# Performance work log

Measured on AMD Instinct MI355X. Metric: run time of the kernel, lower is better.

Reference implementation:

```python
import jax, jax.numpy as jnp
import numpy as np

B, S, D = 16, 2048, 128

def setup_inputs() -> dict:
    key = jax.random.key(0)
    k1, k2, k3, k4 = jax.random.split(key, 4)
    q = jax.random.normal(k1, (B, S, D), dtype=jnp.float32)
    k = jax.random.normal(k2, (B, S, D), dtype=jnp.float32)
    v = jax.random.normal(k3, (B, S, D), dtype=jnp.float32)
    scale = jnp.float32(1.0 / np.sqrt(D))
    attn_mask = jax.random.randint(k4, (B, S, S), 0, 2).astype(jnp.bool_)
    return {"q": q, "k": k, "v": v, "scale": scale, "attn_mask": attn_mask}

def reference(q, k, v, scale, attn_mask):
    # attention scores: [B, Sq, Sk]
    scores = jnp.einsum('bqd,bkd->bqk', q, k) * scale
    # masked_fill(attn_mask, -inf): True positions are masked out
    scores = jnp.where(attn_mask, -jnp.inf, scores)
    attention = jax.nn.softmax(scores, axis=2)
    # dropout prob = 0.0 -> identity
    context = jnp.einsum('bqk,bkd->bqd', attention, v)
    return (context, attention)
```

## Files before the change

kernel.cpp:

```cpp
#include <hip/hip_runtime.h>
#include <hip/hip_bf16.h>
#include <hip/hip_fp16.h>

#define B_ 16
#define S_ 2048
#define D_ 128
#define QB 64
#define KT 64
#define NT_ 32

typedef __attribute__((ext_vector_type(8))) short short8;
typedef __attribute__((ext_vector_type(8))) unsigned short u16x8;
typedef __attribute__((ext_vector_type(4))) float f32x4;
typedef __attribute__((ext_vector_type(4))) float f32x4v;
typedef __attribute__((ext_vector_type(4))) int i32x4;
typedef __attribute__((ext_vector_type(4))) unsigned short u16x4;

__device__ __forceinline__ unsigned short f2bf(float f) {
  unsigned int u = __builtin_bit_cast(unsigned int, f);
  unsigned int r = (u + 0x7fffu + ((u >> 16) & 1u)) >> 16;
  return (unsigned short)r;
}
__device__ __forceinline__ float bf2f(unsigned short h) {
  return __builtin_bit_cast(float, (unsigned int)h << 16);
}
__device__ __forceinline__ int swz_bid(int bid, int nwg) {
  int cpx = nwg >> 3;
  return (bid & 7) * cpx + (bid >> 3);
}

__global__ void cvt_bf16_kernel(const float* __restrict__ x,
                                unsigned short* __restrict__ y,
                                const float* __restrict__ sc, int n4) {
  int i = blockIdx.x * blockDim.x + threadIdx.x;
  if (i >= n4) return;
  float s = sc ? sc[0] : 1.0f;
  float4 f = reinterpret_cast<const float4*>(x)[i];
  u16x4 o;
  o[0] = f2bf(f.x * s); o[1] = f2bf(f.y * s);
  o[2] = f2bf(f.z * s); o[3] = f2bf(f.w * s);
  reinterpret_cast<u16x4*>(y)[i] = o;
}

__global__ void vtrans_kernel(const float* __restrict__ v,
                              unsigned short* __restrict__ vT) {
  __shared__ float tile[32][33];
  int b = blockIdx.z, kt = blockIdx.x, dt = blockIdx.y;
  int t = threadIdx.x;
  int c = t & 31, r0 = t >> 5;
  const float* src = v + ((size_t)b * S_ + (size_t)kt * 32) * D_ + dt * 32;
#pragma unroll
  for (int i = 0; i < 4; i++) {
    int r = r0 + 8 * i;
    tile[r][c] = src[(size_t)r * D_ + c];
  }
  __syncthreads();
  unsigned short* dst = vT + ((size_t)b * D_ + dt * 32) * S_ + (size_t)kt * 32;
#pragma unroll
  for (int i = 0; i < 4; i++) {
    int r = r0 + 8 * i;
    dst[(size_t)r * S_ + c] = f2bf(tile[c][r]);
  }
}

__global__ __launch_bounds__(512, 4)
void attn_main_kernel(const unsigned short* __restrict__ qbf,
                      const unsigned short* __restrict__ kbf,
                      const unsigned short* __restrict__ vTb,
                      const void* __restrict__ maskp,
                      float* __restrict__ ctx,
                      float* __restrict__ att) {
  __shared__ __align__(16) char kbuf[2][KT * 256];
  __shared__ __align__(16) char vbuf[2][D_ * 128];
  __shared__ __align__(16) char etile[QB * 128];
  __shared__ float zpart[8][2][16];
  __shared__ float iz_l[QB];

  const int tid = threadIdx.x;
  const int bid = swz_bid(blockIdx.x, B_ * (S_ / QB));
  const int b  = bid >> 5;
  const int q0 = (bid & 31) << 6;

  const int w   = tid >> 6;
  const int l   = tid & 63;
  const int l16 = l & 15;
  const int lq  = l >> 4;
  const int qh  = w & 1;
  const int kq  = w >> 1;

  int myv = 0;
  if (tid < 256) myv = (reinterpret_cast<const unsigned int*>(maskp)[tid] > 1u) ? 1 : 0;
  const int mask_is_byte = __syncthreads_or(myv);

  const char* kbb = reinterpret_cast<const char*>(kbf + (((size_t)b * S_) << 7));
  const char* vbb = reinterpret_cast<const char*>(vTb + ((size_t)b * D_) * S_);
  const unsigned char* mask8 = reinterpret_cast<const unsigned char*>(maskp);
  const int* mask32 = reinterpret_cast<const int*>(maskp);
  size_t mrowq[2];
#pragma unroll
  for (int qg = 0; qg < 2; ++qg)
    mrowq[qg] = ((size_t)b * S_ + q0 + qh * 32 + qg * 16 + l16) * S_ + kq * 16 + lq * 4;

  short8 qf[2][4];
#pragma unroll
  for (int qg = 0; qg < 2; ++qg) {
    const unsigned short* qp =
        qbf + (((size_t)(b * S_ + q0 + qh * 32 + qg * 16 + l16)) << 7) + lq * 8;
#pragma unroll
    for (int ks = 0; ks < 4; ks++)
      qf[qg][ks] = *reinterpret_cast<const short8*>(qp + ks * 32);
  }

  const int krow_s = tid >> 3, kcol_s = (tid & 7) * 32;
  const int vrow_s = tid >> 2, vcol_s = (tid & 3) * 32;
  const size_t ksrc_off = (size_t)krow_s * 256 + kcol_s;
  const size_t vsrc_off = (size_t)vrow_s * (S_ * 2) + vcol_s;
  const int kswz = (krow_s & 15) << 4, vswz = (vrow_s & 7) << 4;

  u16x8 stk0, stk1, stv0, stv1;
  stk0 = *reinterpret_cast<const u16x8*>(kbb + ksrc_off);
  stk1 = *reinterpret_cast<const u16x8*>(kbb + ksrc_off + 16);
  {
    char* kd = &kbuf[0][0] + krow_s * 256;
    *reinterpret_cast<u16x8*>(kd + (kcol_s ^ kswz)) = stk0;
    *reinterpret_cast<u16x8*>(kd + ((kcol_s + 16) ^ kswz)) = stk1;
  }
  __syncthreads();

  unsigned int mbits[8] = {0, 0, 0, 0, 0, 0, 0, 0};
  float Zl[2] = {0.0f, 0.0f};
  const int krow_f = kq * 16 + l16;
  const int kfx = (krow_f & 15) << 4;

  for (int t = 0; t < NT_; ++t) {
    const int cur = t & 1;
    if (t < NT_ - 1) {
      const char* src = kbb + ((size_t)(t + 1) * KT * 256);
      stk0 = *reinterpret_cast<const u16x8*>(src + ksrc_off);
      stk1 = *reinterpret_cast<const u16x8*>(src + ksrc_off + 16);
    }
    unsigned int nib[2];
    if (mask_is_byte) {
#pragma unroll
      for (int qg = 0; qg < 2; ++qg) {
        unsigned int mv = *reinterpret_cast<const unsigned int*>(
            mask8 + mrowq[qg] + t * KT);
        nib[qg] = ((mv & 0x000000ffu) ? 1u : 0u) | ((mv & 0x0000ff00u) ? 2u : 0u) |
                  ((mv & 0x00ff0000u) ? 4u : 0u) | ((mv & 0xff000000u) ? 8u : 0u);
      }
    } else {
#pragma unroll
      for (int qg = 0; qg < 2; ++qg) {
        i32x4 mi = *reinterpret_cast<const i32x4*>(mask32 + mrowq[qg] + t * KT);
        nib[qg] = (mi[0] ? 1u : 0u) | (mi[1] ? 2u : 0u) |
                  (mi[2] ? 4u : 0u) | (mi[3] ? 8u : 0u);
      }
    }
    mbits[t >> 2] |= (nib[0] | (nib[1] << 4)) << ((t & 3) * 8);

    const char* kp = &kbuf[cur][0] + krow_f * 256;
    f32x4 a0 = {0.f, 0.f, 0.f, 0.f}, a1 = {0.f, 0.f, 0.f, 0.f};
#pragma unroll
    for (int ks = 0; ks < 4; ++ks) {
      short8 kfr = *reinterpret_cast<const short8*>(kp + ((ks * 64 + lq * 16) ^ kfx));
      a0 = __builtin_amdgcn_mfma_f32_16x16x32_bf16(kfr, qf[0][ks], a0, 0, 0, 0);
      a1 = __builtin_amdgcn_mfma_f32_16x16x32_bf16(kfr, qf[1][ks], a1, 0, 0, 0);
    }
#pragma unroll
    for (int r = 0; r < 4; ++r) {
      if (!(nib[0] & (1u << r))) Zl[0] += __expf(a0[r]);
      if (!(nib[1] & (1u << r))) Zl[1] += __expf(a1[r]);
    }
    if (t < NT_ - 1) {
      char* kd = &kbuf[cur ^ 1][0] + krow_s * 256;
      *reinterpret_cast<u16x8*>(kd + (kcol_s ^ kswz)) = stk0;
      *reinterpret_cast<u16x8*>(kd + ((kcol_s + 16) ^ kswz)) = stk1;
    }
    __syncthreads();
  }

  stk0 = *reinterpret_cast<const u16x8*>(kbb + ksrc_off);
  stk1 = *reinterpret_cast<const u16x8*>(kbb + ksrc_off + 16);
  stv0 = *reinterpret_cast<const u16x8*>(vbb + vsrc_off);
  stv1 = *reinterpret_cast<const u16x8*>(vbb + vsrc_off + 16);
#pragma unroll
  for (int qg = 0; qg < 2; ++qg) {
    Zl[qg] += __shfl_xor(Zl[qg], 16, 64);
    Zl[qg] += __shfl_xor(Zl[qg], 32, 64);
  }
  if (lq == 0) { zpart[w][0][l16] = Zl[0]; zpart[w][1][l16] = Zl[1]; }
  __syncthreads();
  if (tid < QB) {
    const int qh_ = tid >> 5, qg_ = (tid >> 4) & 1, r_ = tid & 15;
    float Z = 0.0f;
#pragma unroll
    for (int kk = 0; kk < 4; ++kk) Z += zpart[kk * 2 + qh_][qg_][r_];
    iz_l[tid] = 1.0f / Z;
  }
  {
    char* kd = &kbuf[0][0] + krow_s * 256;
    *reinterpret_cast<u16x8*>(kd + (kcol_s ^ kswz)) = stk0;
    *reinterpret_cast<u16x8*>(kd + ((kcol_s + 16) ^ kswz)) = stk1;
    char* vd = &vbuf[0][0] + vrow_s * 128;
    *reinterpret_cast<u16x8*>(vd + (vcol_s ^ vswz)) = stv0;
    *reinterpret_cast<u16x8*>(vd + ((vcol_s + 16) ^ vswz)) = stv1;
  }
  __syncthreads();

  const float izA = iz_l[w * 8 + (l >> 4)];
  const float izB = iz_l[w * 8 + 4 + (l >> 4)];

  f32x4 apv[2][2] = {{{0.f,0.f,0.f,0.f},{0.f,0.f,0.f,0.f}},
                     {{0.f,0.f,0.f,0.f},{0.f,0.f,0.f,0.f}}};
  for (int t = 0; t < NT_; ++t) {
    const int cur = t & 1;
    if (t < NT_ - 1) {
      const char* src = kbb + ((size_t)(t + 1) * KT * 256);
      stk0 = *reinterpret_cast<const u16x8*>(src + ksrc_off);
      stk1 = *reinterpret_cast<const u16x8*>(src + ksrc_off + 16);
      const char* vs2 = vbb + (size_t)(t + 1) * 128;
      stv0 = *reinterpret_cast<const u16x8*>(vs2 + vsrc_off);
      stv1 = *reinterpret_cast<const u16x8*>(vs2 + vsrc_off + 16);
    }
    const char* kp = &kbuf[cur][0] + krow_f * 256;
    f32x4 a0 = {0.f, 0.f, 0.f, 0.f}, a1 = {0.f, 0.f, 0.f, 0.f};
#pragma unroll
    for (int ks = 0; ks < 4; ++ks) {
      short8 kfr = *reinterpret_cast<const short8*>(kp + ((ks * 64 + lq * 16) ^ kfx));
      a0 = __builtin_amdgcn_mfma_f32_16x16x32_bf16(kfr, qf[0][ks], a0, 0, 0, 0);
      a1 = __builtin_amdgcn_mfma_f32_16x16x32_bf16(kfr, qf[1][ks], a1, 0, 0, 0);
    }
    const unsigned int nibs = mbits[t >> 2] >> ((t & 3) * 8);
    u16x4 eb[2];
#pragma unroll
    for (int r = 0; r < 4; ++r) {
      eb[0][r] = f2bf((nibs & (1u << r)) ? 0.0f : __expf(a0[r]));
      eb[1][r] = f2bf((nibs & (16u << r)) ? 0.0f : __expf(a1[r]));
    }
    __syncthreads();
#pragma unroll
    for (int qg = 0; qg < 2; ++qg) {
      const int re = qh * 32 + qg * 16 + l16;
      *reinterpret_cast<u16x4*>(
          etile + re * 128 + ((kq * 32 + lq * 8) ^ ((re & 7) << 4))) = eb[qg];
    }
    if (t < NT_ - 1) {
      char* kd = &kbuf[cur ^ 1][0] + krow_s * 256;
      *reinterpret_cast<u16x8*>(kd + (kcol_s ^ kswz)) = stk0;
      *reinterpret_cast<u16x8*>(kd + ((kcol_s + 16) ^ kswz)) = stk1;
      char* vd = &vbuf[cur ^ 1][0] + vrow_s * 128;
      *reinterpret_cast<u16x8*>(vd + (vcol_s ^ vswz)) = stv0;
      *reinterpret_cast<u16x8*>(vd + ((vcol_s + 16) ^ vswz)) = stv1;
    }
    __syncthreads();
#pragma unroll
    for (int h = 0; h < 2; ++h) {
      const int re = w * 8 + h * 4 + (l >> 4);
      const float iz = h ? izB : izA;
      u16x4 ev = *reinterpret_cast<const u16x4*>(
          etile + re * 128 + (((l & 15) * 8) ^ ((re & 7) << 4)));
      f32x4v pv;
#pragma unroll
      for (int j = 0; j < 4; ++j) pv[j] = bf2f(ev[j]) * iz;
      __builtin_nontemporal_store(pv, reinterpret_cast<f32x4v*>(
          att + ((size_t)(b * S_ + q0 + re)) * S_ + t * KT + (l & 15) * 4));
    }
#pragma unroll
    for (int qg = 0; qg < 2; ++qg) {
      const int re = qh * 32 + qg * 16 + l16;
      const char* ep = etile + re * 128;
      const int ex = (re & 7) << 4;
#pragma unroll
      for (int dg = 0; dg < 2; ++dg) {
        const int vr = kq * 32 + dg * 16 + l16;
        const char* vp = &vbuf[cur][0] + vr * 128;
        const int vx = (vr & 7) << 4;
#pragma unroll
        for (int kk = 0; kk < 2; ++kk) {
          short8 afr = *reinterpret_cast<const short8*>(ep + ((kk * 64 + lq * 16) ^ ex));
          short8 bfr = *reinterpret_cast<const short8*>(vp + ((kk * 64 + lq * 16) ^ vx));
          apv[qg][dg] = __builtin_amdgcn_mfma_f32_16x16x32_bf16(afr, bfr, apv[qg][dg], 0, 0, 0);
        }
      }
    }
  }

#pragma unroll
  for (int qg = 0; qg < 2; ++qg) {
#pragma unroll
    for (int dg = 0; dg < 2; ++dg) {
#pragma unroll
      for (int r = 0; r < 4; ++r) {
        const float izr = iz_l[qh * 32 + qg * 16 + lq * 4 + r];
        __builtin_nontemporal_store(
            apv[qg][dg][r] * izr,
            ctx + ((size_t)(b * S_ + q0 + qh * 32 + qg * 16 + lq * 4 + r)) * D_ +
                kq * 32 + dg * 16 + l16);
      }
    }
  }
}

extern "C" void kernel_launch(void* const* d_in, const int* in_sizes, int n_in,
                              void* d_out, int out_size, void* d_ws, size_t ws_size,
                              hipStream_t stream) {
  (void)in_sizes; (void)n_in; (void)out_size; (void)ws_size;
  const float* q = (const float*)d_in[0];
  const float* k = (const float*)d_in[1];
  const float* v = (const float*)d_in[2];
  const float* scale = (const float*)d_in[3];
  const void* mask = d_in[4];

  const size_t qkv_elems = (size_t)B_ * S_ * D_;
  unsigned short* qbf = (unsigned short*)d_ws;
  unsigned short* kbf = qbf + qkv_elems;
  unsigned short* vTb = kbf + qkv_elems;

  float* ctx = (float*)d_out;
  float* att = ctx + (size_t)B_ * S_ * D_;

  const int n4 = B_ * S_ * D_ / 4;
  cvt_bf16_kernel<<<dim3((n4 + 255) / 256), dim3(256), 0, stream>>>(q, qbf, scale, n4);
  cvt_bf16_kernel<<<dim3((n4 + 255) / 256), dim3(256), 0, stream>>>(k, kbf, nullptr, n4);
  vtrans_kernel<<<dim3(S_ / 32, D_ / 32, B_), dim3(256), 0, stream>>>(v, vTb);
  attn_main_kernel<<<dim3(B_ * (S_ / QB)), dim3(512), 0, stream>>>(
      qbf, kbf, vTb, mask, ctx, att);
}
```

Before: 162.7 us.

## Precompute packed mask bits and load K/V fragments directly from global

Adds a separate kernel that packs the boolean mask into 64-bit nibble words per query row and key tile, so the main kernel reads compact bits instead of the raw mask on each pass. The main kernel halves the query block to 32 rows with 256 threads and drops the LDS staging of K and V. Each wave now loads its MFMA fragments straight from global memory with register prefetch. Normalization moves into the exp step before bf16 rounding, which removes the per-store scaling of context. The trade-off is a lower-bandwidth mask read against redundant global loads of K and V, an extra kernel launch and extra workspace use.

```diff
diff --git a/kernel.cpp b/kernel.cpp
--- a/kernel.cpp
+++ b/kernel.cpp
@@ -5,7 +5,7 @@
 #define B_ 16
 #define S_ 2048
 #define D_ 128
-#define QB 64
+#define QB 32
 #define KT 64
 #define NT_ 32
 
@@ -63,126 +63,117 @@
   }
 }
 
-__global__ __launch_bounds__(512, 4)
+__global__ void masknib_kernel(const void* __restrict__ maskp,
+                               unsigned long long* __restrict__ mnib) {
+  const int tid = threadIdx.x;
+  int myv = (reinterpret_cast<const unsigned int*>(maskp)[tid] > 1u) ? 1 : 0;
+  const int mask_is_byte = __syncthreads_or(myv);
+  const size_t i = (size_t)blockIdx.x * 256 + tid;
+  const int t = i & 31;
+  const int q = (i >> 5) & 2047;
+  const int b = i >> 16;
+  const size_t base = ((size_t)(b * S_ + q)) * S_ + t * 64;
+  unsigned long long out = 0;
+  if (mask_is_byte) {
+    const unsigned char* m8 = reinterpret_cast<const unsigned char*>(maskp) + base;
+#pragma unroll
+    for (int c4 = 0; c4 < 16; ++c4) {
+      unsigned int v = *reinterpret_cast<const unsigned int*>(m8 + c4 * 4);
+      unsigned long long nib = ((v & 0x000000ffu) ? 1u : 0u) |
+                               ((v & 0x0000ff00u) ? 2u : 0u) |
+                               ((v & 0x00ff0000u) ? 4u : 0u) |
+                               ((v & 0xff000000u) ? 8u : 0u);
+      out |= nib << (4 * c4);
+    }
+  } else {
+    const int* m32 = reinterpret_cast<const int*>(maskp) + base;
+#pragma unroll
+    for (int c4 = 0; c4 < 16; ++c4) {
+      i32x4 mi = *reinterpret_cast<const i32x4*>(m32 + c4 * 4);
+      unsigned long long nib = (mi[0] ? 1u : 0u) | (mi[1] ? 2u : 0u) |
+                               (mi[2] ? 4u : 0u) | (mi[3] ? 8u : 0u);
+      out |= nib << (4 * c4);
+    }
+  }
+  mnib[i] = out;
+}
+
+__global__ __launch_bounds__(256, 4)
 void attn_main_kernel(const unsigned short* __restrict__ qbf,
                       const unsigned short* __restrict__ kbf,
                       const unsigned short* __restrict__ vTb,
-                      const void* __restrict__ maskp,
+                      const unsigned long long* __restrict__ mnib,
                       float* __restrict__ ctx,
                       float* __restrict__ att) {
-  __shared__ __align__(16) char kbuf[2][KT * 256];
-  __shared__ __align__(16) char vbuf[2][D_ * 128];
   __shared__ __align__(16) char etile[QB * 128];
-  __shared__ float zpart[8][2][16];
+  __shared__ float zpart[4][2][16];
   __shared__ float iz_l[QB];
 
   const int tid = threadIdx.x;
   const int bid = swz_bid(blockIdx.x, B_ * (S_ / QB));
-  const int b  = bid >> 5;
-  const int q0 = (bid & 31) << 6;
+  const int b  = bid >> 6;
+  const int q0 = (bid & 63) << 5;
 
   const int w   = tid >> 6;
   const int l   = tid & 63;
   const int l16 = l & 15;
   const int lq  = l >> 4;
-  const int qh  = w & 1;
-  const int kq  = w >> 1;
-
-  int myv = 0;
-  if (tid < 256) myv = (reinterpret_cast<const unsigned int*>(maskp)[tid] > 1u) ? 1 : 0;
-  const int mask_is_byte = __syncthreads_or(myv);
-
-  const char* kbb = reinterpret_cast<const char*>(kbf + (((size_t)b * S_) << 7));
-  const char* vbb = reinterpret_cast<const char*>(vTb + ((size_t)b * D_) * S_);
-  const unsigned char* mask8 = reinterpret_cast<const unsigned char*>(maskp);
-  const int* mask32 = reinterpret_cast<const int*>(maskp);
-  size_t mrowq[2];
-#pragma unroll
-  for (int qg = 0; qg < 2; ++qg)
-    mrowq[qg] = ((size_t)b * S_ + q0 + qh * 32 + qg * 16 + l16) * S_ + kq * 16 + lq * 4;
 
   short8 qf[2][4];
 #pragma unroll
   for (int qg = 0; qg < 2; ++qg) {
     const unsigned short* qp =
-        qbf + (((size_t)(b * S_ + q0 + qh * 32 + qg * 16 + l16)) << 7) + lq * 8;
+        qbf + (((size_t)(b * S_ + q0 + qg * 16 + l16)) << 7) + lq * 8;
 #pragma unroll
     for (int ks = 0; ks < 4; ks++)
       qf[qg][ks] = *reinterpret_cast<const short8*>(qp + ks * 32);
   }
 
-  const int krow_s = tid >> 3, kcol_s = (tid & 7) * 32;
-  const int vrow_s = tid >> 2, vcol_s = (tid & 3) * 32;
-  const size_t ksrc_off = (size_t)krow_s * 256 + kcol_s;
-  const size_t vsrc_off = (size_t)vrow_s * (S_ * 2) + vcol_s;
-  const int kswz = (krow_s & 15) << 4, vswz = (vrow_s & 7) << 4;
-
-  u16x8 stk0, stk1, stv0, stv1;
-  stk0 = *reinterpret_cast<const u16x8*>(kbb + ksrc_off);
-  stk1 = *reinterpret_cast<const u16x8*>(kbb + ksrc_off + 16);
+  const unsigned long long* mp0 =
+      mnib + ((size_t)(b * S_ + q0 + l16)) * NT_;
+  const unsigned long long* mp1 =
+      mnib + ((size_t)(b * S_ + q0 + 16 + l16)) * NT_;
+  const int nsh = (w * 4 + lq) * 4;
+
+  const char* kbb = reinterpret_cast<const char*>(kbf) + ((size_t)b * S_) * 256;
+  const char* vbb = reinterpret_cast<const char*>(vTb) + ((size_t)b * D_) * (S_ * 2);
+
+  short8 kc[4], kn[4];
   {
-    char* kd = &kbuf[0][0] + krow_s * 256;
-    *reinterpret_cast<u16x8*>(kd + (kcol_s ^ kswz)) = stk0;
-    *reinterpret_cast<u16x8*>(kd + ((kcol_s + 16) ^ kswz)) = stk1;
-  }
-  __syncthreads();
-
-  unsigned int mbits[8] = {0, 0, 0, 0, 0, 0, 0, 0};
+    const char* kp = kbb + ((size_t)(w * 16 + l16)) * 256 + lq * 16;
+#pragma unroll
+    for (int ks = 0; ks < 4; ++ks)
+      kc[ks] = *reinterpret_cast<const short8*>(kp + ks * 64);
+  }
+  unsigned long long mc0 = mp0[0], mc1 = mp1[0], mn0, mn1;
   float Zl[2] = {0.0f, 0.0f};
-  const int krow_f = kq * 16 + l16;
-  const int kfx = (krow_f & 15) << 4;
-
   for (int t = 0; t < NT_; ++t) {
-    const int cur = t & 1;
-    if (t < NT_ - 1) {
-      const char* src = kbb + ((size_t)(t + 1) * KT * 256);
-      stk0 = *reinterpret_cast<const u16x8*>(src + ksrc_off);
-      stk1 = *reinterpret_cast<const u16x8*>(src + ksrc_off + 16);
-    }
-    unsigned int nib[2];
-    if (mask_is_byte) {
-#pragma unroll
-      for (int qg = 0; qg < 2; ++qg) {
-        unsigned int mv = *reinterpret_cast<const unsigned int*>(
-            mask8 + mrowq[qg] + t * KT);
-        nib[qg] = ((mv & 0x000000ffu) ? 1u : 0u) | ((mv & 0x0000ff00u) ? 2u : 0u) |
-                  ((mv & 0x00ff0000u) ? 4u : 0u) | ((mv & 0xff000000u) ? 8u : 0u);
-      }
-    } else {
-#pragma unroll
-      for (int qg = 0; qg < 2; ++qg) {
-        i32x4 mi = *reinterpret_cast<const i32x4*>(mask32 + mrowq[qg] + t * KT);
-        nib[qg] = (mi[0] ? 1u : 0u) | (mi[1] ? 2u : 0u) |
-                  (mi[2] ? 4u : 0u) | (mi[3] ? 8u : 0u);
-      }
-    }
-    mbits[t >> 2] |= (nib[0] | (nib[1] << 4)) << ((t & 3) * 8);
-
-    const char* kp = &kbuf[cur][0] + krow_f * 256;
+    if (t + 1 < NT_) {
+      const char* kp = kbb + ((size_t)((t + 1) * KT + w * 16 + l16)) * 256 + lq * 16;
+#pragma unroll
+      for (int ks = 0; ks < 4; ++ks)
+        kn[ks] = *reinterpret_cast<const short8*>(kp + ks * 64);
+      mn0 = mp0[t + 1];
+      mn1 = mp1[t + 1];
+    }
     f32x4 a0 = {0.f, 0.f, 0.f, 0.f}, a1 = {0.f, 0.f, 0.f, 0.f};
 #pragma unroll
     for (int ks = 0; ks < 4; ++ks) {
-      short8 kfr = *reinterpret_cast<const short8*>(kp + ((ks * 64 + lq * 16) ^ kfx));
-      a0 = __builtin_amdgcn_mfma_f32_16x16x32_bf16(kfr, qf[0][ks], a0, 0, 0, 0);
-      a1 = __builtin_amdgcn_mfma_f32_16x16x32_bf16(kfr, qf[1][ks], a1, 0, 0, 0);
-    }
+      a0 = __builtin_amdgcn_mfma_f32_16x16x32_bf16(kc[ks], qf[0][ks], a0, 0, 0, 0);
+      a1 = __builtin_amdgcn_mfma_f32_16x16x32_bf16(kc[ks], qf[1][ks], a1, 0, 0, 0);
+    }
+    const unsigned int n0 = (unsigned int)(mc0 >> nsh) & 15u;
+    const unsigned int n1 = (unsigned int)(mc1 >> nsh) & 15u;
 #pragma unroll
     for (int r = 0; r < 4; ++r) {
-      if (!(nib[0] & (1u << r))) Zl[0] += __expf(a0[r]);
-      if (!(nib[1] & (1u << r))) Zl[1] += __expf(a1[r]);
-    }
-    if (t < NT_ - 1) {
-      char* kd = &kbuf[cur ^ 1][0] + krow_s * 256;
-      *reinterpret_cast<u16x8*>(kd + (kcol_s ^ kswz)) = stk0;
-      *reinterpret_cast<u16x8*>(kd + ((kcol_s + 16) ^ kswz)) = stk1;
-    }
-    __syncthreads();
-  }
-
-  stk0 = *reinterpret_cast<const u16x8*>(kbb + ksrc_off);
-  stk1 = *reinterpret_cast<const u16x8*>(kbb + ksrc_off + 16);
-  stv0 = *reinterpret_cast<const u16x8*>(vbb + vsrc_off);
-  stv1 = *reinterpret_cast<const u16x8*>(vbb + vsrc_off + 16);
+      if (!((n0 >> r) & 1u)) Zl[0] += __expf(a0[r]);
+      if (!((n1 >> r) & 1u)) Zl[1] += __expf(a1[r]);
+    }
+#pragma unroll
+    for (int ks = 0; ks < 4; ++ks) kc[ks] = kn[ks];
+    mc0 = mn0; mc1 = mn1;
+  }
+
 #pragma unroll
   for (int qg = 0; qg < 2; ++qg) {
     Zl[qg] += __shfl_xor(Zl[qg], 16, 64);
@@ -191,98 +182,93 @@
   if (lq == 0) { zpart[w][0][l16] = Zl[0]; zpart[w][1][l16] = Zl[1]; }
   __syncthreads();
   if (tid < QB) {
-    const int qh_ = tid >> 5, qg_ = (tid >> 4) & 1, r_ = tid & 15;
-    float Z = 0.0f;
-#pragma unroll
-    for (int kk = 0; kk < 4; ++kk) Z += zpart[kk * 2 + qh_][qg_][r_];
+    const int qg_ = tid >> 4, r_ = tid & 15;
+    float Z = zpart[0][qg_][r_] + zpart[1][qg_][r_] +
+              zpart[2][qg_][r_] + zpart[3][qg_][r_];
     iz_l[tid] = 1.0f / Z;
   }
-  {
-    char* kd = &kbuf[0][0] + krow_s * 256;
-    *reinterpret_cast<u16x8*>(kd + (kcol_s ^ kswz)) = stk0;
-    *reinterpret_cast<u16x8*>(kd + ((kcol_s + 16) ^ kswz)) = stk1;
-    char* vd = &vbuf[0][0] + vrow_s * 128;
-    *reinterpret_cast<u16x8*>(vd + (vcol_s ^ vswz)) = stv0;
-    *reinterpret_cast<u16x8*>(vd + ((vcol_s + 16) ^ vswz)) = stv1;
-  }
   __syncthreads();
-
-  const float izA = iz_l[w * 8 + (l >> 4)];
-  const float izB = iz_l[w * 8 + 4 + (l >> 4)];
+  const float izq0 = iz_l[l16];
+  const float izq1 = iz_l[16 + l16];
 
   f32x4 apv[2][2] = {{{0.f,0.f,0.f,0.f},{0.f,0.f,0.f,0.f}},
                      {{0.f,0.f,0.f,0.f},{0.f,0.f,0.f,0.f}}};
+  {
+    const char* kp = kbb + ((size_t)(w * 16 + l16)) * 256 + lq * 16;
+#pragma unroll
+    for (int ks = 0; ks < 4; ++ks)
+      kc[ks] = *reinterpret_cast<const short8*>(kp + ks * 64);
+  }
+  mc0 = mp0[0]; mc1 = mp1[0];
   for (int t = 0; t < NT_; ++t) {
-    const int cur = t & 1;
-    if (t < NT_ - 1) {
-      const char* src = kbb + ((size_t)(t + 1) * KT * 256);
-      stk0 = *reinterpret_cast<const u16x8*>(src + ksrc_off);
-      stk1 = *reinterpret_cast<const u16x8*>(src + ksrc_off + 16);
-      const char* vs2 = vbb + (size_t)(t + 1) * 128;
-      stv0 = *reinterpret_cast<const u16x8*>(vs2 + vsrc_off);
-      stv1 = *reinterpret_cast<const u16x8*>(vs2 + vsrc_off + 16);
-    }
-    const char* kp = &kbuf[cur][0] + krow_f * 256;
+    short8 bv[2][2];
+#pragma unroll
+    for (int dg = 0; dg < 2; ++dg) {
+      const char* vp = vbb + ((size_t)(w * 32 + dg * 16 + l16)) * (S_ * 2)
+                           + (t * 64 + lq * 8) * 2;
+#pragma unroll
+      for (int kk = 0; kk < 2; ++kk)
+        bv[dg][kk] = *reinterpret_cast<const short8*>(vp + kk * 64);
+    }
+    if (t + 1 < NT_) {
+      const char* kp = kbb + ((size_t)((t + 1) * KT + w * 16 + l16)) * 256 + lq * 16;
+#pragma unroll
+      for (int ks = 0; ks < 4; ++ks)
+        kn[ks] = *reinterpret_cast<const short8*>(kp + ks * 64);
+      mn0 = mp0[t + 1];
+      mn1 = mp1[t + 1];
+    }
     f32x4 a0 = {0.f, 0.f, 0.f, 0.f}, a1 = {0.f, 0.f, 0.f, 0.f};
 #pragma unroll
     for (int ks = 0; ks < 4; ++ks) {
-      short8 kfr = *reinterpret_cast<const short8*>(kp + ((ks * 64 + lq * 16) ^ kfx));
-      a0 = __builtin_amdgcn_mfma_f32_16x16x32_bf16(kfr, qf[0][ks], a0, 0, 0, 0);
-      a1 = __builtin_amdgcn_mfma_f32_16x16x32_bf16(kfr, qf[1][ks], a1, 0, 0, 0);
-    }
-    const unsigned int nibs = mbits[t >> 2] >> ((t & 3) * 8);
-    u16x4 eb[2];
+      a0 = __builtin_amdgcn_mfma_f32_16x16x32_bf16(kc[ks], qf[0][ks], a0, 0, 0, 0);
+      a1 = __builtin_amdgcn_mfma_f32_16x16x32_bf16(kc[ks], qf[1][ks], a1, 0, 0, 0);
+    }
+    const unsigned int n0 = (unsigned int)(mc0 >> nsh) & 15u;
+    const unsigned int n1 = (unsigned int)(mc1 >> nsh) & 15u;
+    u16x4 eb0, eb1;
 #pragma unroll
     for (int r = 0; r < 4; ++r) {
-      eb[0][r] = f2bf((nibs & (1u << r)) ? 0.0f : __expf(a0[r]));
-      eb[1][r] = f2bf((nibs & (16u << r)) ? 0.0f : __expf(a1[r]));
+      float p0 = ((n0 >> r) & 1u) ? 0.0f : __expf(a0[r]) * izq0;
+      float p1 = ((n1 >> r) & 1u) ? 0.0f : __expf(a1[r]) * izq1;
+      eb0[r] = f2bf(p0);
+      eb1[r] = f2bf(p1);
     }
     __syncthreads();
+    {
+      const int c = w * 32 + lq * 8;
+      const int r0_ = l16, r1_ = 16 + l16;
+      *reinterpret_cast<u16x4*>(etile + r0_ * 128 + (c ^ ((r0_ & 7) << 4))) = eb0;
+      *reinterpret_cast<u16x4*>(etile + r1_ * 128 + (c ^ ((r1_ & 7) << 4))) = eb1;
+    }
+    __syncthreads();
+    {
+      const int re = w * 8 + (l >> 3);
+      const int cb = (l & 7) * 16;
+      u16x8 ev = *reinterpret_cast<const u16x8*>(
+          etile + re * 128 + (cb ^ ((re & 7) << 4)));
+      f32x4v o0, o1;
+#pragma unroll
+      for (int j = 0; j < 4; ++j) { o0[j] = bf2f(ev[j]); o1[j] = bf2f(ev[j + 4]); }
+      float* ap = att + ((size_t)(b * S_ + q0 + re)) * S_ + t * 64 + (l & 7) * 8;
+      __builtin_nontemporal_store(o0, reinterpret_cast<f32x4v*>(ap));
+      __builtin_nontemporal_store(o1, reinterpret_cast<f32x4v*>(ap) + 1);
+    }
 #pragma unroll
     for (int qg = 0; qg < 2; ++qg) {
-      const int re = qh * 32 + qg * 16 + l16;
-      *reinterpret_cast<u16x4*>(
-          etile + re * 128 + ((kq * 32 + lq * 8) ^ ((re & 7) << 4))) = eb[qg];
-    }
-    if (t < NT_ - 1) {
-      char* kd = &kbuf[cur ^ 1][0] + krow_s * 256;
-      *reinterpret_cast<u16x8*>(kd + (kcol_s ^ kswz)) = stk0;
-      *reinterpret_cast<u16x8*>(kd + ((kcol_s + 16) ^ kswz)) = stk1;
-      char* vd = &vbuf[cur ^ 1][0] + vrow_s * 128;
-      *reinterpret_cast<u16x8*>(vd + (vcol_s ^ vswz)) = stv0;
-      *reinterpret_cast<u16x8*>(vd + ((vcol_s + 16) ^ vswz)) = stv1;
-    }
-    __syncthreads();
-#pragma unroll
-    for (int h = 0; h < 2; ++h) {
-      const int re = w * 8 + h * 4 + (l >> 4);
-      const float iz = h ? izB : izA;
-      u16x4 ev = *reinterpret_cast<const u16x4*>(
-          etile + re * 128 + (((l & 15) * 8) ^ ((re & 7) << 4)));
-      f32x4v pv;
-#pragma unroll
-      for (int j = 0; j < 4; ++j) pv[j] = bf2f(ev[j]) * iz;
-      __builtin_nontemporal_store(pv, reinterpret_cast<f32x4v*>(
-          att + ((size_t)(b * S_ + q0 + re)) * S_ + t * KT + (l & 15) * 4));
-    }
-#pragma unroll
-    for (int qg = 0; qg < 2; ++qg) {
-      const int re = qh * 32 + qg * 16 + l16;
-      const char* ep = etile + re * 128;
-      const int ex = (re & 7) << 4;
-#pragma unroll
-      for (int dg = 0; dg < 2; ++dg) {
-        const int vr = kq * 32 + dg * 16 + l16;
-        const char* vp = &vbuf[cur][0] + vr * 128;
-        const int vx = (vr & 7) << 4;
-#pragma unroll
-        for (int kk = 0; kk < 2; ++kk) {
-          short8 afr = *reinterpret_cast<const short8*>(ep + ((kk * 64 + lq * 16) ^ ex));
-          short8 bfr = *reinterpret_cast<const short8*>(vp + ((kk * 64 + lq * 16) ^ vx));
-          apv[qg][dg] = __builtin_amdgcn_mfma_f32_16x16x32_bf16(afr, bfr, apv[qg][dg], 0, 0, 0);
-        }
+      const int rq = qg * 16 + l16;
+      const char* ep = etile + rq * 128;
+      const int ex = (rq & 7) << 4;
+#pragma unroll
+      for (int kk = 0; kk < 2; ++kk) {
+        short8 afr = *reinterpret_cast<const short8*>(ep + ((kk * 64 + lq * 16) ^ ex));
+        apv[qg][0] = __builtin_amdgcn_mfma_f32_16x16x32_bf16(afr, bv[0][kk], apv[qg][0], 0, 0, 0);
+        apv[qg][1] = __builtin_amdgcn_mfma_f32_16x16x32_bf16(afr, bv[1][kk], apv[qg][1], 0, 0, 0);
       }
     }
+#pragma unroll
+    for (int ks = 0; ks < 4; ++ks) kc[ks] = kn[ks];
+    mc0 = mn0; mc1 = mn1;
   }
 
 #pragma unroll
@@ -291,11 +277,10 @@
     for (int dg = 0; dg < 2; ++dg) {
 #pragma unroll
       for (int r = 0; r < 4; ++r) {
-        const float izr = iz_l[qh * 32 + qg * 16 + lq * 4 + r];
         __builtin_nontemporal_store(
-            apv[qg][dg][r] * izr,
-            ctx + ((size_t)(b * S_ + q0 + qh * 32 + qg * 16 + lq * 4 + r)) * D_ +
-                kq * 32 + dg * 16 + l16);
+            apv[qg][dg][r],
+            ctx + ((size_t)(b * S_ + q0 + qg * 16 + lq * 4 + r)) * D_ +
+                w * 32 + dg * 16 + l16);
       }
     }
   }
@@ -315,6 +300,8 @@
   unsigned short* qbf = (unsigned short*)d_ws;
   unsigned short* kbf = qbf + qkv_elems;
   unsigned short* vTb = kbf + qkv_elems;
+  unsigned long long* mnib =
+      (unsigned long long*)(vTb + qkv_elems);
 
   float* ctx = (float*)d_out;
   float* att = ctx + (size_t)B_ * S_ * D_;
@@ -323,6 +310,7 @@
   cvt_bf16_kernel<<<dim3((n4 + 255) / 256), dim3(256), 0, stream>>>(q, qbf, scale, n4);
   cvt_bf16_kernel<<<dim3((n4 + 255) / 256), dim3(256), 0, stream>>>(k, kbf, nullptr, n4);
   vtrans_kernel<<<dim3(S_ / 32, D_ / 32, B_), dim3(256), 0, stream>>>(v, vTb);
-  attn_main_kernel<<<dim3(B_ * (S_ / QB)), dim3(512), 0, stream>>>(
-      qbf, kbf, vTb, mask, ctx, att);
-}
+  masknib_kernel<<<dim3(B_ * S_ * NT_ / 256), dim3(256), 0, stream>>>(mask, mnib);
+  attn_main_kernel<<<dim3(B_ * (S_ / QB)), dim3(256), 0, stream>>>(
+      qbf, kbf, vTb, mnib, ctx, att);
+}
```

Result: slower. 345.0 us (+112.1%).

## Precompute packed mask bits in a separate kernel and fold normalization into exp

Applied to the files above, without the earlier changes.

A new pre-pass kernel reads the boolean mask once and packs it into 64-bit bitmasks, one per query row and key tile, stored in workspace. The main kernel then loads one 64-bit word per row per tile in both passes instead of reading raw mask bytes, and drops the per-thread mbits register array. The inverse normalizer is now applied before the bf16 rounding of the exponentials, so the attention-matrix store and the context epilogue no longer scale. This costs an extra kernel launch and a 16 MB bitmask round trip, in exchange for lighter mask traffic and lower register use in the main kernel. Rounding after scaling also changes numerics slightly.

```diff
diff --git a/kernel.cpp b/kernel.cpp
--- a/kernel.cpp
+++ b/kernel.cpp
@@ -63,11 +63,46 @@
   }
 }
 
+__global__ void masknib_kernel(const void* __restrict__ maskp,
+                               unsigned long long* __restrict__ mnib) {
+  const int tid = threadIdx.x;
+  int myv = (reinterpret_cast<const unsigned int*>(maskp)[tid] > 1u) ? 1 : 0;
+  const int mask_is_byte = __syncthreads_or(myv);
+  const size_t i = (size_t)blockIdx.x * 256 + tid;
+  const int t = i & 31;
+  const int q = (i >> 5) & 2047;
+  const int b = i >> 16;
+  const size_t base = ((size_t)(b * S_ + q)) * S_ + t * 64;
+  unsigned long long out = 0;
+  if (mask_is_byte) {
+    const unsigned char* m8 = reinterpret_cast<const unsigned char*>(maskp) + base;
+#pragma unroll
+    for (int c4 = 0; c4 < 16; ++c4) {
+      unsigned int v = *reinterpret_cast<const unsigned int*>(m8 + c4 * 4);
+      unsigned long long nib = ((v & 0x000000ffu) ? 1u : 0u) |
+                               ((v & 0x0000ff00u) ? 2u : 0u) |
+                               ((v & 0x00ff0000u) ? 4u : 0u) |
+                               ((v & 0xff000000u) ? 8u : 0u);
+      out |= nib << (4 * c4);
+    }
+  } else {
+    const int* m32 = reinterpret_cast<const int*>(maskp) + base;
+#pragma unroll
+    for (int c4 = 0; c4 < 16; ++c4) {
+      i32x4 mi = *reinterpret_cast<const i32x4*>(m32 + c4 * 4);
+      unsigned long long nib = (mi[0] ? 1u : 0u) | (mi[1] ? 2u : 0u) |
+                               (mi[2] ? 4u : 0u) | (mi[3] ? 8u : 0u);
+      out |= nib << (4 * c4);
+    }
+  }
+  mnib[i] = out;
+}
+
 __global__ __launch_bounds__(512, 4)
 void attn_main_kernel(const unsigned short* __restrict__ qbf,
                       const unsigned short* __restrict__ kbf,
                       const unsigned short* __restrict__ vTb,
-                      const void* __restrict__ maskp,
+                      const unsigned long long* __restrict__ mnib,
                       float* __restrict__ ctx,
                       float* __restrict__ att) {
   __shared__ __align__(16) char kbuf[2][KT * 256];
@@ -88,19 +123,6 @@
   const int qh  = w & 1;
   const int kq  = w >> 1;
 
-  int myv = 0;
-  if (tid < 256) myv = (reinterpret_cast<const unsigned int*>(maskp)[tid] > 1u) ? 1 : 0;
-  const int mask_is_byte = __syncthreads_or(myv);
-
-  const char* kbb = reinterpret_cast<const char*>(kbf + (((size_t)b * S_) << 7));
-  const char* vbb = reinterpret_cast<const char*>(vTb + ((size_t)b * D_) * S_);
-  const unsigned char* mask8 = reinterpret_cast<const unsigned char*>(maskp);
-  const int* mask32 = reinterpret_cast<const int*>(maskp);
-  size_t mrowq[2];
-#pragma unroll
-  for (int qg = 0; qg < 2; ++qg)
-    mrowq[qg] = ((size_t)b * S_ + q0 + qh * 32 + qg * 16 + l16) * S_ + kq * 16 + lq * 4;
-
   short8 qf[2][4];
 #pragma unroll
   for (int qg = 0; qg < 2; ++qg) {
@@ -110,6 +132,15 @@
     for (int ks = 0; ks < 4; ks++)
       qf[qg][ks] = *reinterpret_cast<const short8*>(qp + ks * 32);
   }
+
+  const unsigned long long* mp0 =
+      mnib + ((size_t)(b * S_ + q0 + qh * 32 + l16)) * NT_;
+  const unsigned long long* mp1 =
+      mnib + ((size_t)(b * S_ + q0 + qh * 32 + 16 + l16)) * NT_;
+  const int nsh = kq * 16 + lq * 4;
+
+  const char* kbb = reinterpret_cast<const char*>(kbf + (((size_t)b * S_) << 7));
+  const char* vbb = reinterpret_cast<const char*>(vTb + ((size_t)b * D_) * S_);
 
   const int krow_s = tid >> 3, kcol_s = (tid & 7) * 32;
   const int vrow_s = tid >> 2, vcol_s = (tid & 3) * 32;
@@ -127,10 +158,10 @@
   }
   __syncthreads();
 
-  unsigned int mbits[8] = {0, 0, 0, 0, 0, 0, 0, 0};
   float Zl[2] = {0.0f, 0.0f};
   const int krow_f = kq * 16 + l16;
   const int kfx = (krow_f & 15) << 4;
+  unsigned long long mc0 = mp0[0], mc1 = mp1[0], mn0 = 0, mn1 = 0;
 
   for (int t = 0; t < NT_; ++t) {
     const int cur = t & 1;
@@ -138,26 +169,9 @@
       const char* src = kbb + ((size_t)(t + 1) * KT * 256);
       stk0 = *reinterpret_cast<const u16x8*>(src + ksrc_off);
       stk1 = *reinterpret_cast<const u16x8*>(src + ksrc_off + 16);
-    }
-    unsigned int nib[2];
-    if (mask_is_byte) {
-#pragma unroll
-      for (int qg = 0; qg < 2; ++qg) {
-        unsigned int mv = *reinterpret_cast<const unsigned int*>(
-            mask8 + mrowq[qg] + t * KT);
-        nib[qg] = ((mv & 0x000000ffu) ? 1u : 0u) | ((mv & 0x0000ff00u) ? 2u : 0u) |
-                  ((mv & 0x00ff0000u) ? 4u : 0u) | ((mv & 0xff000000u) ? 8u : 0u);
-      }
-    } else {
-#pragma unroll
-      for (int qg = 0; qg < 2; ++qg) {
-        i32x4 mi = *reinterpret_cast<const i32x4*>(mask32 + mrowq[qg] + t * KT);
-        nib[qg] = (mi[0] ? 1u : 0u) | (mi[1] ? 2u : 0u) |
-                  (mi[2] ? 4u : 0u) | (mi[3] ? 8u : 0u);
-      }
-    }
-    mbits[t >> 2] |= (nib[0] | (nib[1] << 4)) << ((t & 3) * 8);
-
+      mn0 = mp0[t + 1];
+      mn1 = mp1[t + 1];
+    }
     const char* kp = &kbuf[cur][0] + krow_f * 256;
     f32x4 a0 = {0.f, 0.f, 0.f, 0.f}, a1 = {0.f, 0.f, 0.f, 0.f};
 #pragma unroll
@@ -166,16 +180,19 @@
       a0 = __builtin_amdgcn_mfma_f32_16x16x32_bf16(kfr, qf[0][ks], a0, 0, 0, 0);
       a1 = __builtin_amdgcn_mfma_f32_16x16x32_bf16(kfr, qf[1][ks], a1, 0, 0, 0);
     }
+    const unsigned int n0 = (unsigned int)(mc0 >> nsh) & 15u;
+    const unsigned int n1 = (unsigned int)(mc1 >> nsh) & 15u;
 #pragma unroll
     for (int r = 0; r < 4; ++r) {
-      if (!(nib[0] & (1u << r))) Zl[0] += __expf(a0[r]);
-      if (!(nib[1] & (1u << r))) Zl[1] += __expf(a1[r]);
+      if (!((n0 >> r) & 1u)) Zl[0] += __expf(a0[r]);
+      if (!((n1 >> r) & 1u)) Zl[1] += __expf(a1[r]);
     }
     if (t < NT_ - 1) {
       char* kd = &kbuf[cur ^ 1][0] + krow_s * 256;
       *reinterpret_cast<u16x8*>(kd + (kcol_s ^ kswz)) = stk0;
       *reinterpret_cast<u16x8*>(kd + ((kcol_s + 16) ^ kswz)) = stk1;
     }
+    mc0 = mn0; mc1 = mn1;
     __syncthreads();
   }
 
@@ -207,11 +224,12 @@
   }
   __syncthreads();
 
-  const float izA = iz_l[w * 8 + (l >> 4)];
-  const float izB = iz_l[w * 8 + 4 + (l >> 4)];
+  const float izq0 = iz_l[qh * 32 + l16];
+  const float izq1 = iz_l[qh * 32 + 16 + l16];
 
   f32x4 apv[2][2] = {{{0.f,0.f,0.f,0.f},{0.f,0.f,0.f,0.f}},
                      {{0.f,0.f,0.f,0.f},{0.f,0.f,0.f,0.f}}};
+  mc0 = mp0[0]; mc1 = mp1[0];
   for (int t = 0; t < NT_; ++t) {
     const int cur = t & 1;
     if (t < NT_ - 1) {
@@ -221,6 +239,8 @@
       const char* vs2 = vbb + (size_t)(t + 1) * 128;
       stv0 = *reinterpret_cast<const u16x8*>(vs2 + vsrc_off);
       stv1 = *reinterpret_cast<const u16x8*>(vs2 + vsrc_off + 16);
+      mn0 = mp0[t + 1];
+      mn1 = mp1[t + 1];
     }
     const char* kp = &kbuf[cur][0] + krow_f * 256;
     f32x4 a0 = {0.f, 0.f, 0.f, 0.f}, a1 = {0.f, 0.f, 0.f, 0.f};
@@ -230,12 +250,13 @@
       a0 = __builtin_amdgcn_mfma_f32_16x16x32_bf16(kfr, qf[0][ks], a0, 0, 0, 0);
       a1 = __builtin_amdgcn_mfma_f32_16x16x32_bf16(kfr, qf[1][ks], a1, 0, 0, 0);
     }
-    const unsigned int nibs = mbits[t >> 2] >> ((t & 3) * 8);
+    const unsigned int n0 = (unsigned int)(mc0 >> nsh) & 15u;
+    const unsigned int n1 = (unsigned int)(mc1 >> nsh) & 15u;
     u16x4 eb[2];
 #pragma unroll
     for (int r = 0; r < 4; ++r) {
-      eb[0][r] = f2bf((nibs & (1u << r)) ? 0.0f : __expf(a0[r]));
-      eb[1][r] = f2bf((nibs & (16u << r)) ? 0.0f : __expf(a1[r]));
+      eb[0][r] = f2bf(((n0 >> r) & 1u) ? 0.0f : __expf(a0[r]) * izq0);
+      eb[1][r] = f2bf(((n1 >> r) & 1u) ? 0.0f : __expf(a1[r]) * izq1);
     }
     __syncthreads();
 #pragma unroll
@@ -252,16 +273,16 @@
       *reinterpret_cast<u16x8*>(vd + (vcol_s ^ vswz)) = stv0;
       *reinterpret_cast<u16x8*>(vd + ((vcol_s + 16) ^ vswz)) = stv1;
     }
+    mc0 = mn0; mc1 = mn1;
     __syncthreads();
 #pragma unroll
     for (int h = 0; h < 2; ++h) {
       const int re = w * 8 + h * 4 + (l >> 4);
-      const float iz = h ? izB : izA;
       u16x4 ev = *reinterpret_cast<const u16x4*>(
           etile + re * 128 + (((l & 15) * 8) ^ ((re & 7) << 4)));
       f32x4v pv;
 #pragma unroll
-      for (int j = 0; j < 4; ++j) pv[j] = bf2f(ev[j]) * iz;
+      for (int j = 0; j < 4; ++j) pv[j] = bf2f(ev[j]);
       __builtin_nontemporal_store(pv, reinterpret_cast<f32x4v*>(
           att + ((size_t)(b * S_ + q0 + re)) * S_ + t * KT + (l & 15) * 4));
     }
@@ -291,9 +312,8 @@
     for (int dg = 0; dg < 2; ++dg) {
 #pragma unroll
       for (int r = 0; r < 4; ++r) {
-        const float izr = iz_l[qh * 32 + qg * 16 + lq * 4 + r];
         __builtin_nontemporal_store(
-            apv[qg][dg][r] * izr,
+            apv[qg][dg][r],
             ctx + ((size_t)(b * S_ + q0 + qh * 32 + qg * 16 + lq * 4 + r)) * D_ +
                 kq * 32 + dg * 16 + l16);
       }
@@ -315,6 +335,8 @@
   unsigned short* qbf = (unsigned short*)d_ws;
   unsigned short* kbf = qbf + qkv_elems;
   unsigned short* vTb = kbf + qkv_elems;
+  unsigned long long* mnib =
+      (unsigned long long*)(vTb + qkv_elems);
 
   float* ctx = (float*)d_out;
   float* att = ctx + (size_t)B_ * S_ * D_;
@@ -323,6 +345,7 @@
   cvt_bf16_kernel<<<dim3((n4 + 255) / 256), dim3(256), 0, stream>>>(q, qbf, scale, n4);
   cvt_bf16_kernel<<<dim3((n4 + 255) / 256), dim3(256), 0, stream>>>(k, kbf, nullptr, n4);
   vtrans_kernel<<<dim3(S_ / 32, D_ / 32, B_), dim3(256), 0, stream>>>(v, vTb);
+  masknib_kernel<<<dim3(B_ * S_ * NT_ / 256), dim3(256), 0, stream>>>(mask, mnib);
   attn_main_kernel<<<dim3(B_ * (S_ / QB)), dim3(512), 0, stream>>>(
-      qbf, kbf, vTb, mask, ctx, att);
-}
+      qbf, kbf, vTb, mnib, ctx, att);
+}
```

New measurement: 207.8 us. 1.28x slower.

## Fold log2e into Q, normalize before PV, add MFMA priority hints

Applied to the files above, without the earlier changes.

Multiplies log2(e) into the Q conversion scale so the kernel can use the hardware exp2 instead of __expf. It also applies 1/Z before the bf16 rounding of probabilities, which removes the separate rescale of the attention tile and the final context rescale. It regroups the PV MFMA loop so fragments are loaded first and then issued back to back, and brackets MFMA blocks with s_setprio. The cost is a slight change in where rounding happens and some added register pressure from holding the fragments.

```diff
diff --git a/kernel.cpp b/kernel.cpp
--- a/kernel.cpp
+++ b/kernel.cpp
@@ -8,6 +8,7 @@
 #define QB 64
 #define KT 64
 #define NT_ 32
+#define LOG2E 1.4426950408889634f
 
 typedef __attribute__((ext_vector_type(8))) short short8;
 typedef __attribute__((ext_vector_type(8))) unsigned short u16x8;
@@ -16,6 +17,9 @@
 typedef __attribute__((ext_vector_type(4))) int i32x4;
 typedef __attribute__((ext_vector_type(4))) unsigned short u16x4;
 
+__device__ __forceinline__ float exp2fast(float x) {
+  return __builtin_amdgcn_exp2f(x);
+}
 __device__ __forceinline__ unsigned short f2bf(float f) {
   unsigned int u = __builtin_bit_cast(unsigned int, f);
   unsigned int r = (u + 0x7fffu + ((u >> 16) & 1u)) >> 16;
@@ -31,10 +35,11 @@
 
 __global__ void cvt_bf16_kernel(const float* __restrict__ x,
                                 unsigned short* __restrict__ y,
-                                const float* __restrict__ sc, int n4) {
+                                const float* __restrict__ sc, float postmul,
+                                int n4) {
   int i = blockIdx.x * blockDim.x + threadIdx.x;
   if (i >= n4) return;
-  float s = sc ? sc[0] : 1.0f;
+  float s = (sc ? sc[0] : 1.0f) * postmul;
   float4 f = reinterpret_cast<const float4*>(x)[i];
   u16x4 o;
   o[0] = f2bf(f.x * s); o[1] = f2bf(f.y * s);
@@ -92,8 +97,16 @@
   if (tid < 256) myv = (reinterpret_cast<const unsigned int*>(maskp)[tid] > 1u) ? 1 : 0;
   const int mask_is_byte = __syncthreads_or(myv);
 
-  const char* kbb = reinterpret_cast<const char*>(kbf + (((size_t)b * S_) << 7));
-  const char* vbb = reinterpret_cast<const char*>(vTb + ((size_t)b * D_) * S_);
+  short8 qf[2][4];
+#pragma unroll
+  for (int qg = 0; qg < 2; ++qg) {
+    const unsigned short* qp =
+        qbf + (((size_t)(b * S_ + q0 + qh * 32 + qg * 16 + l16)) << 7) + lq * 8;
+#pragma unroll
+    for (int ks = 0; ks < 4; ks++)
+      qf[qg][ks] = *reinterpret_cast<const short8*>(qp + ks * 32);
+  }
+
   const unsigned char* mask8 = reinterpret_cast<const unsigned char*>(maskp);
   const int* mask32 = reinterpret_cast<const int*>(maskp);
   size_t mrowq[2];
@@ -101,15 +114,8 @@
   for (int qg = 0; qg < 2; ++qg)
     mrowq[qg] = ((size_t)b * S_ + q0 + qh * 32 + qg * 16 + l16) * S_ + kq * 16 + lq * 4;
 
-  short8 qf[2][4];
-#pragma unroll
-  for (int qg = 0; qg < 2; ++qg) {
-    const unsigned short* qp =
-        qbf + (((size_t)(b * S_ + q0 + qh * 32 + qg * 16 + l16)) << 7) + lq * 8;
-#pragma unroll
-    for (int ks = 0; ks < 4; ks++)
-      qf[qg][ks] = *reinterpret_cast<const short8*>(qp + ks * 32);
-  }
+  const char* kbb = reinterpret_cast<const char*>(kbf + (((size_t)b * S_) << 7));
+  const char* vbb = reinterpret_cast<const char*>(vTb + ((size_t)b * D_) * S_);
 
   const int krow_s = tid >> 3, kcol_s = (tid & 7) * 32;
   const int vrow_s = tid >> 2, vcol_s = (tid & 3) * 32;
@@ -160,16 +166,18 @@
 
     const char* kp = &kbuf[cur][0] + krow_f * 256;
     f32x4 a0 = {0.f, 0.f, 0.f, 0.f}, a1 = {0.f, 0.f, 0.f, 0.f};
+    __builtin_amdgcn_s_setprio(1);
 #pragma unroll
     for (int ks = 0; ks < 4; ++ks) {
       short8 kfr = *reinterpret_cast<const short8*>(kp + ((ks * 64 + lq * 16) ^ kfx));
       a0 = __builtin_amdgcn_mfma_f32_16x16x32_bf16(kfr, qf[0][ks], a0, 0, 0, 0);
       a1 = __builtin_amdgcn_mfma_f32_16x16x32_bf16(kfr, qf[1][ks], a1, 0, 0, 0);
     }
+    __builtin_amdgcn_s_setprio(0);
 #pragma unroll
     for (int r = 0; r < 4; ++r) {
-      if (!(nib[0] & (1u << r))) Zl[0] += __expf(a0[r]);
-      if (!(nib[1] & (1u << r))) Zl[1] += __expf(a1[r]);
+      if (!((nib[0] >> r) & 1u)) Zl[0] += exp2fast(a0[r]);
+      if (!((nib[1] >> r) & 1u)) Zl[1] += exp2fast(a1[r]);
     }
     if (t < NT_ - 1) {
       char* kd = &kbuf[cur ^ 1][0] + krow_s * 256;
@@ -207,8 +215,8 @@
   }
   __syncthreads();
 
-  const float izA = iz_l[w * 8 + (l >> 4)];
-  const float izB = iz_l[w * 8 + 4 + (l >> 4)];
+  const float izq0 = iz_l[qh * 32 + l16];
+  const float izq1 = iz_l[qh * 32 + 16 + l16];
 
   f32x4 apv[2][2] = {{{0.f,0.f,0.f,0.f},{0.f,0.f,0.f,0.f}},
                      {{0.f,0.f,0.f,0.f},{0.f,0.f,0.f,0.f}}};
@@ -224,18 +232,20 @@
     }
     const char* kp = &kbuf[cur][0] + krow_f * 256;
     f32x4 a0 = {0.f, 0.f, 0.f, 0.f}, a1 = {0.f, 0.f, 0.f, 0.f};
+    __builtin_amdgcn_s_setprio(1);
 #pragma unroll
     for (int ks = 0; ks < 4; ++ks) {
       short8 kfr = *reinterpret_cast<const short8*>(kp + ((ks * 64 + lq * 16) ^ kfx));
       a0 = __builtin_amdgcn_mfma_f32_16x16x32_bf16(kfr, qf[0][ks], a0, 0, 0, 0);
       a1 = __builtin_amdgcn_mfma_f32_16x16x32_bf16(kfr, qf[1][ks], a1, 0, 0, 0);
     }
+    __builtin_amdgcn_s_setprio(0);
     const unsigned int nibs = mbits[t >> 2] >> ((t & 3) * 8);
     u16x4 eb[2];
 #pragma unroll
     for (int r = 0; r < 4; ++r) {
-      eb[0][r] = f2bf((nibs & (1u << r)) ? 0.0f : __expf(a0[r]));
-      eb[1][r] = f2bf((nibs & (16u << r)) ? 0.0f : __expf(a1[r]));
+      eb[0][r] = f2bf((nibs & (1u << r)) ? 0.0f : exp2fast(a0[r]) * izq0);
+      eb[1][r] = f2bf((nibs & (16u << r)) ? 0.0f : exp2fast(a1[r]) * izq1);
     }
     __syncthreads();
 #pragma unroll
@@ -256,32 +266,37 @@
 #pragma unroll
     for (int h = 0; h < 2; ++h) {
       const int re = w * 8 + h * 4 + (l >> 4);
-      const float iz = h ? izB : izA;
       u16x4 ev = *reinterpret_cast<const u16x4*>(
           etile + re * 128 + (((l & 15) * 8) ^ ((re & 7) << 4)));
       f32x4v pv;
 #pragma unroll
-      for (int j = 0; j < 4; ++j) pv[j] = bf2f(ev[j]) * iz;
+      for (int j = 0; j < 4; ++j) pv[j] = bf2f(ev[j]);
       __builtin_nontemporal_store(pv, reinterpret_cast<f32x4v*>(
           att + ((size_t)(b * S_ + q0 + re)) * S_ + t * KT + (l & 15) * 4));
     }
 #pragma unroll
-    for (int qg = 0; qg < 2; ++qg) {
-      const int re = qh * 32 + qg * 16 + l16;
-      const char* ep = etile + re * 128;
-      const int ex = (re & 7) << 4;
+    for (int kk = 0; kk < 2; ++kk) {
+      short8 afr[2], bfr[2];
+#pragma unroll
+      for (int qg = 0; qg < 2; ++qg) {
+        const int re = qh * 32 + qg * 16 + l16;
+        afr[qg] = *reinterpret_cast<const short8*>(
+            etile + re * 128 + ((kk * 64 + lq * 16) ^ ((re & 7) << 4)));
+      }
 #pragma unroll
       for (int dg = 0; dg < 2; ++dg) {
         const int vr = kq * 32 + dg * 16 + l16;
-        const char* vp = &vbuf[cur][0] + vr * 128;
-        const int vx = (vr & 7) << 4;
-#pragma unroll
-        for (int kk = 0; kk < 2; ++kk) {
-          short8 afr = *reinterpret_cast<const short8*>(ep + ((kk * 64 + lq * 16) ^ ex));
-          short8 bfr = *reinterpret_cast<const short8*>(vp + ((kk * 64 + lq * 16) ^ vx));
-          apv[qg][dg] = __builtin_amdgcn_mfma_f32_16x16x32_bf16(afr, bfr, apv[qg][dg], 0, 0, 0);
-        }
-      }
+        bfr[dg] = *reinterpret_cast<const short8*>(
+            &vbuf[cur][0] + vr * 128 + ((kk * 64 + lq * 16) ^ ((vr & 7) << 4)));
+      }
+      __builtin_amdgcn_s_setprio(1);
+#pragma unroll
+      for (int qg = 0; qg < 2; ++qg)
+#pragma unroll
+        for (int dg = 0; dg < 2; ++dg)
+          apv[qg][dg] = __builtin_amdgcn_mfma_f32_16x16x32_bf16(
+              afr[qg], bfr[dg], apv[qg][dg], 0, 0, 0);
+      __builtin_amdgcn_s_setprio(0);
     }
   }
 
@@ -291,9 +306,8 @@
     for (int dg = 0; dg < 2; ++dg) {
 #pragma unroll
       for (int r = 0; r < 4; ++r) {
-        const float izr = iz_l[qh * 32 + qg * 16 + lq * 4 + r];
         __builtin_nontemporal_store(
-            apv[qg][dg][r] * izr,
+            apv[qg][dg][r],
             ctx + ((size_t)(b * S_ + q0 + qh * 32 + qg * 16 + lq * 4 + r)) * D_ +
                 kq * 32 + dg * 16 + l16);
       }
@@ -320,8 +334,10 @@
   float* att = ctx + (size_t)B_ * S_ * D_;
 
   const int n4 = B_ * S_ * D_ / 4;
-  cvt_bf16_kernel<<<dim3((n4 + 255) / 256), dim3(256), 0, stream>>>(q, qbf, scale, n4);
-  cvt_bf16_kernel<<<dim3((n4 + 255) / 256), dim3(256), 0, stream>>>(k, kbf, nullptr, n4);
+  cvt_bf16_kernel<<<dim3((n4 + 255) / 256), dim3(256), 0, stream>>>(
+      q, qbf, scale, LOG2E, n4);
+  cvt_bf16_kernel<<<dim3((n4 + 255) / 256), dim3(256), 0, stream>>>(
+      k, kbf, nullptr, 1.0f, n4);
   vtrans_kernel<<<dim3(S_ / 32, D_ / 32, B_), dim3(256), 0, stream>>>(v, vTb);
   attn_main_kernel<<<dim3(B_ * (S_ / QB)), dim3(512), 0, stream>>>(
       qbf, kbf, vTb, mask, ctx, att);
```

Measured after the change: 162.8 us. Within noise of the previous version (+0.1%).
